# Optimization experiments

Hardware: AMD Instinct MI355X
Metric: run time of the kernel (lower is better)

Reference implementation:

```python
import jax, jax.numpy as jnp
import numpy as np

INPUT_DIM = 384
H1, H2, BOTTLENECK = 512, 216, 10
NUM_ANNOTATORS = 2316
BATCH = 16384


def setup_inputs() -> dict:
    key = jax.random.key(0)
    ks = jax.random.split(key, 9)

    def lin(k, fan_in, fan_out):
        # torch nn.Linear default init: U(-1/sqrt(fan_in), 1/sqrt(fan_in))
        bound = 1.0 / np.sqrt(fan_in)
        kw, kb = jax.random.split(k)
        W = jax.random.uniform(kw, (fan_in, fan_out), jnp.float32, -bound, bound)
        b = jax.random.uniform(kb, (fan_out,), jnp.float32, -bound, bound)
        return W, b

    x = jax.random.normal(ks[0], (BATCH, INPUT_DIM), jnp.float32)
    W1, b1 = lin(ks[1], INPUT_DIM, H1)
    W2, b2 = lin(ks[2], H1, H2)
    W3, b3 = lin(ks[3], H2, BOTTLENECK)
    # 2316 heads of Linear(10, 1) stacked into a single (10, 2316) matrix + (2316,) bias
    Wh, bh = lin(ks[4], BOTTLENECK, NUM_ANNOTATORS)
    return {"x": x, "W1": W1, "b1": b1, "W2": W2, "b2": b2,
            "W3": W3, "b3": b3, "Wh": Wh, "bh": bh}


def reference(x, W1, b1, W2, b2, W3, b3, Wh, bh):
    # shared encoder (dropout is identity in eval mode)
    h = jax.nn.relu(x @ W1 + b1)            # [B, 512]
    h = jax.nn.relu(h @ W2 + b2)            # [B, 216]
    f = jax.nn.relu(h @ W3 + b3)            # [B, 10]
    # 2316 per-annotator heads fused into one GEMM: [B,10] @ [10,2316] + [2316]
    return f @ Wh + bh                      # [B, 2316]
```

## Files before the change

### kernel.cpp

```cpp
#include <hip/hip_runtime.h>
#include <hip/hip_bf16.h>
#include <stdint.h>

using f32x4  = __attribute__((ext_vector_type(4))) float;
using bf16x8 = __attribute__((ext_vector_type(8))) __bf16;
using u16x4  = __attribute__((ext_vector_type(4))) unsigned short;
using u16x8  = __attribute__((ext_vector_type(8))) unsigned short;

#define DEVFN static __device__ __forceinline__

constexpr int IND = 384, N1 = 512, N2R = 216, N2 = 256, NB = 10, NA = 2316;
constexpr int BATCH = 16384;
constexpr int RB  = 64;
constexpr int NC1 = 12;
constexpr int NC2 = 16;
constexpr int K3  = 224;

constexpr int WS_W1  = 0;
constexpr int WS_W2  = WS_W1 + NC1 * N1 * 32;
constexpr int WS_W3  = WS_W2 + NC2 * N2 * 32;
constexpr size_t WS_NEED = 708864;

constexpr int XT_OFF = 0;      constexpr int XT_ST = 784;
constexpr int W1T    = 51200;
constexpr int H1_OFF = 0;      constexpr int H1_ST = 1040;
constexpr int W2T    = 66560;
constexpr int H2_OFF = 0;      constexpr int H2_ST = 528;
constexpr int W3_OFF = 115712;
constexpr int F_OFF  = 122880; constexpr int F_ST  = 48;
constexpr int B1L    = 149504;
constexpr int B2L    = 151552;
constexpr int B3L    = 152576;
constexpr int LDS_E  = 152640;

DEVFN unsigned short bf16u(float f) {
    __hip_bfloat16 h = __float2bfloat16(f);
    unsigned short u; __builtin_memcpy(&u, &h, 2); return u;
}

DEVFN void mfma16(f32x4& d, bf16x8 a, bf16x8 b) {
    d = __builtin_amdgcn_mfma_f32_16x16x32_bf16(a, b, d, 0, 0, 0);
}

DEVFN void gll16(const void* g, void* lds) {
    __builtin_amdgcn_global_load_lds((const __attribute__((address_space(1))) void*)g,
                                     (__attribute__((address_space(3))) void*)lds, 16, 0, 0);
}

DEVFN void wait_vm4()   { asm volatile("s_waitcnt vmcnt(4)" ::: "memory"); }
DEVFN void wait_vm2()   { asm volatile("s_waitcnt vmcnt(2)" ::: "memory"); }
DEVFN void wait_vm0()   { asm volatile("s_waitcnt vmcnt(0)" ::: "memory"); }
DEVFN void wait_lgkm0() { asm volatile("s_waitcnt lgkmcnt(0)" ::: "memory"); }

__global__ __launch_bounds__(256)
void cvt_weights(const float* __restrict__ W1, const float* __restrict__ W2,
                 const float* __restrict__ W3,
                 unsigned short* __restrict__ ws)
{
    const int bid = blockIdx.x, tid = threadIdx.x;
    if (bid < 48) {
        const int c = bid >> 2, o = bid & 3;
        #pragma unroll
        for (int half = 0; half < 2; ++half) {
            const int col = half * 256 + tid;
            u16x8 v;
            #pragma unroll
            for (int s7 = 0; s7 < 8; ++s7)
                v[s7] = bf16u(W1[(size_t)(c * 32 + o * 8 + s7) * N1 + col]);
            *(u16x8*)(ws + WS_W1 + c * 16384 + col * 32 + ((o ^ (col & 3)) << 3)) = v;
        }
    } else if (bid < 112) {
        const int t = bid - 48;
        const int c = t >> 2, o = t & 3;
        const int col = tid;
        u16x8 v;
        #pragma unroll
        for (int s7 = 0; s7 < 8; ++s7) {
            int k = c * 32 + o * 8 + s7;
            v[s7] = (col < N2R) ? bf16u(W2[(size_t)k * N2R + col]) : (unsigned short)0;
        }
        *(u16x8*)(ws + WS_W2 + c * 8192 + col * 32 + ((o ^ (col & 3)) << 3)) = v;
    } else {
        for (int i = tid; i < 16 * K3; i += 256) {
            int col = i / K3, s = i - col * K3;
            int sb = s >> 5, r = s & 31;
            int k = sb * 32 + (((r >> 3) ^ (col & 3)) << 3) + (r & 7);
            float v = (col < NB && k < 216) ? W3[k * NB + col] : 0.f;
            ws[WS_W3 + i] = bf16u(v);
        }
    }
}

__global__ __launch_bounds__(512)
void fused_mlp(const float* __restrict__ x,
               const float* __restrict__ b1g, const float* __restrict__ b2g,
               const float* __restrict__ b3g,
               const unsigned short* __restrict__ ws,
               const float* __restrict__ WhG, const float* __restrict__ bhg,
               float* __restrict__ out)
{
    __shared__ __attribute__((aligned(16))) unsigned char smem[LDS_E];
    const int tid  = threadIdx.x;
    const int wave = tid >> 6;
    const int lane = tid & 63;
    const int l16  = lane & 15;
    const int lk   = lane >> 4;
    const int wr   = wave >> 2;
    const int wc   = wave & 3;
    const int row0 = blockIdx.x * RB;

    const unsigned char* wsW1 = (const unsigned char*)(ws + WS_W1);
    const unsigned char* wsW2 = (const unsigned char*)(ws + WS_W2);

    #pragma unroll
    for (int cc = 0; cc < 2; ++cc)
        #pragma unroll
        for (int o = 0; o < 4; ++o) {
            int wb = o * 8192 + wave * 1024;
            gll16(wsW1 + cc * 32768 + wb + lane * 16, smem + W1T + cc * 32768 + wb);
        }

    {
        const float4* xg = (const float4*)(x + (size_t)row0 * IND);
        #pragma unroll
        for (int i = 0; i < 12; ++i) {
            int j = tid + i * 512;
            float4 v = xg[j];
            int el = j * 4, r = el / IND, c = el - r * IND;
            u16x4 h;
            h[0] = bf16u(v.x); h[1] = bf16u(v.y); h[2] = bf16u(v.z); h[3] = bf16u(v.w);
            *(u16x4*)(smem + XT_OFF + r * XT_ST + c * 2) = h;
        }
        *(float*)(smem + B1L + tid * 4) = b1g[tid];
        if (tid < 256) *(float*)(smem + B2L + tid * 4) = (tid < N2R) ? b2g[tid] : 0.f;
        if (tid < 16)  *(float*)(smem + B3L + tid * 4) = (tid < NB)  ? b3g[tid] : 0.f;
    }
    __syncthreads();

    f32x4 acc1[2][8] = {};

    for (int c = 0; c < NC1; ++c) {
        if (c + 1 < NC1) wait_vm4(); else wait_vm2();
        __builtin_amdgcn_s_barrier();
        if (c + 2 < NC1) {
            const unsigned char* src = wsW1 + (size_t)(c + 2) * 32768;
            const int nxt = W1T + ((c + 2) % 3) * 32768;
            #pragma unroll
            for (int o = 0; o < 4; ++o) {
                int wb = o * 8192 + wave * 1024;
                gll16(src + wb + lane * 16, smem + nxt + wb);
            }
        } else {
            const int cc = c - 10;
            #pragma unroll
            for (int o = 0; o < 2; ++o) {
                int wb = o * 8192 + wave * 1024;
                gll16(wsW2 + cc * 16384 + wb + lane * 16, smem + W2T + cc * 16384 + wb);
            }
        }
        const int cur = W1T + (c % 3) * 32768;
        const int k0 = c * 32;
        bf16x8 a0 = *(const bf16x8*)(smem + XT_OFF + (wr * 32 + l16)      * XT_ST + (k0 + lk * 8) * 2);
        bf16x8 a1 = *(const bf16x8*)(smem + XT_OFF + (wr * 32 + 16 + l16) * XT_ST + (k0 + lk * 8) * 2);
        #pragma unroll
        for (int n = 0; n < 8; ++n) {
            int col = wc * 128 + n * 16 + l16;
            bf16x8 b = *(const bf16x8*)(smem + cur + col * 64 + ((lk ^ (col & 3)) << 4));
            mfma16(acc1[0][n], a0, b);
            mfma16(acc1[1][n], a1, b);
        }
    }
    __builtin_amdgcn_s_barrier();
    #pragma unroll
    for (int m = 0; m < 2; ++m)
        #pragma unroll
        for (int n = 0; n < 8; ++n) {
            int col = wc * 128 + n * 16 + l16;
            float bias = *(const float*)(smem + B1L + col * 4);
            #pragma unroll
            for (int e = 0; e < 4; ++e) {
                float v = fmaxf(acc1[m][n][e] + bias, 0.f);
                *(unsigned short*)(smem + H1_OFF + (wr * 32 + m * 16 + lk * 4 + e) * H1_ST + col * 2) = bf16u(v);
            }
        }
    wait_lgkm0();
    __builtin_amdgcn_s_barrier();

    f32x4 acc2[2][4] = {};

    for (int c = 0; c < NC2; ++c) {
        if (c + 1 < NC2) wait_vm2(); else wait_vm0();
        __builtin_amdgcn_s_barrier();
        if (c + 2 < NC2) {
            const unsigned char* src = wsW2 + (size_t)(c + 2) * 16384;
            const int nxt = W2T + ((c + 2) % 3) * 16384;
            #pragma unroll
            for (int o = 0; o < 2; ++o) {
                int wb = o * 8192 + wave * 1024;
                gll16(src + wb + lane * 16, smem + nxt + wb);
            }
        }
        const int cur = W2T + (c % 3) * 16384;
        const int k0 = c * 32;
        bf16x8 a0 = *(const bf16x8*)(smem + H1_OFF + (wr * 32 + l16)      * H1_ST + (k0 + lk * 8) * 2);
        bf16x8 a1 = *(const bf16x8*)(smem + H1_OFF + (wr * 32 + 16 + l16) * H1_ST + (k0 + lk * 8) * 2);
        #pragma unroll
        for (int n = 0; n < 4; ++n) {
            int col = wc * 64 + n * 16 + l16;
            bf16x8 b = *(const bf16x8*)(smem + cur + col * 64 + ((lk ^ (col & 3)) << 4));
            mfma16(acc2[0][n], a0, b);
            mfma16(acc2[1][n], a1, b);
        }
    }

    const int j0 = tid;
    const int j1 = 512 + tid;
    const bool has1 = (j1 < 579);
    float w0[10][4], w1[10][4];
    float4 bh0 = ((const float4*)bhg)[j0];
    float4 bh1 = make_float4(0.f, 0.f, 0.f, 0.f);
    #pragma unroll
    for (int k = 0; k < 10; ++k) {
        f32x4 q = *(const f32x4*)(WhG + (size_t)k * NA + j0 * 4);
        w0[k][0] = q[0]; w0[k][1] = q[1]; w0[k][2] = q[2]; w0[k][3] = q[3];
    }
    if (has1) {
        #pragma unroll
        for (int k = 0; k < 10; ++k) {
            f32x4 q = *(const f32x4*)(WhG + (size_t)k * NA + j1 * 4);
            w1[k][0] = q[0]; w1[k][1] = q[1]; w1[k][2] = q[2]; w1[k][3] = q[3];
        }
        bh1 = ((const float4*)bhg)[j1];
    }

    __builtin_amdgcn_s_barrier();
    #pragma unroll
    for (int m = 0; m < 2; ++m)
        #pragma unroll
        for (int n = 0; n < 4; ++n) {
            int col = wc * 64 + n * 16 + l16;
            float bias = *(const float*)(smem + B2L + col * 4);
            #pragma unroll
            for (int e = 0; e < 4; ++e) {
                float v = fmaxf(acc2[m][n][e] + bias, 0.f);
                *(unsigned short*)(smem + H2_OFF + (wr * 32 + m * 16 + lk * 4 + e) * H2_ST + col * 2) = bf16u(v);
            }
        }
    if (wave < 7)
        gll16((const unsigned char*)(ws + WS_W3) + wave * 1024 + lane * 16, smem + W3_OFF + wave * 1024);
    __syncthreads();

    f32x4 acc3[2] = {};
    #pragma unroll
    for (int c = 0; c < 7; ++c) {
        const int k0 = c * 32;
        bf16x8 a0 = *(const bf16x8*)(smem + H2_OFF + (wr * 32 + l16)      * H2_ST + (k0 + lk * 8) * 2);
        bf16x8 a1 = *(const bf16x8*)(smem + H2_OFF + (wr * 32 + 16 + l16) * H2_ST + (k0 + lk * 8) * 2);
        bf16x8 b  = *(const bf16x8*)(smem + W3_OFF + l16 * 448 + c * 64 + ((lk ^ (l16 & 3)) << 4));
        mfma16(acc3[0], a0, b);
        mfma16(acc3[1], a1, b);
    }
    if (wc == 0 && l16 < NB) {
        float bias = *(const float*)(smem + B3L + l16 * 4);
        #pragma unroll
        for (int m = 0; m < 2; ++m)
            #pragma unroll
            for (int e = 0; e < 4; ++e) {
                float v = fmaxf(acc3[m][e] + bias, 0.f);
                *(float*)(smem + F_OFF + (wr * 32 + m * 16 + lk * 4 + e) * F_ST + l16 * 4) = v;
            }
    }
    __syncthreads();

    #pragma unroll 1
    for (int rg = 0; rg < 16; ++rg) {
        float fv[4][10];
        #pragma unroll
        for (int rr = 0; rr < 4; ++rr) {
            const unsigned char* fb = smem + F_OFF + (rg * 4 + rr) * F_ST;
            f32x4 p0 = *(const f32x4*)(fb);
            f32x4 p1 = *(const f32x4*)(fb + 16);
            float2 p2 = *(const float2*)(fb + 32);
            fv[rr][0] = p0[0]; fv[rr][1] = p0[1]; fv[rr][2] = p0[2]; fv[rr][3] = p0[3];
            fv[rr][4] = p1[0]; fv[rr][5] = p1[1]; fv[rr][6] = p1[2]; fv[rr][7] = p1[3];
            fv[rr][8] = p2.x;  fv[rr][9] = p2.y;
        }
        float ac[4][4];
        #pragma unroll
        for (int rr = 0; rr < 4; ++rr) {
            ac[rr][0] = bh0.x; ac[rr][1] = bh0.y; ac[rr][2] = bh0.z; ac[rr][3] = bh0.w;
            #pragma unroll
            for (int k = 0; k < 10; ++k) {
                ac[rr][0] = fmaf(fv[rr][k], w0[k][0], ac[rr][0]);
                ac[rr][1] = fmaf(fv[rr][k], w0[k][1], ac[rr][1]);
                ac[rr][2] = fmaf(fv[rr][k], w0[k][2], ac[rr][2]);
                ac[rr][3] = fmaf(fv[rr][k], w0[k][3], ac[rr][3]);
            }
        }
        #pragma unroll
        for (int rr = 0; rr < 4; ++rr) {
            float4 o;
            o.x = ac[rr][0]; o.y = ac[rr][1]; o.z = ac[rr][2]; o.w = ac[rr][3];
            *(float4*)(out + (size_t)(row0 + rg * 4 + rr) * NA + j0 * 4) = o;
        }
        if (has1) {
            float ac1[4][4];
            #pragma unroll
            for (int rr = 0; rr < 4; ++rr) {
                ac1[rr][0] = bh1.x; ac1[rr][1] = bh1.y; ac1[rr][2] = bh1.z; ac1[rr][3] = bh1.w;
                #pragma unroll
                for (int k = 0; k < 10; ++k) {
                    ac1[rr][0] = fmaf(fv[rr][k], w1[k][0], ac1[rr][0]);
                    ac1[rr][1] = fmaf(fv[rr][k], w1[k][1], ac1[rr][1]);
                    ac1[rr][2] = fmaf(fv[rr][k], w1[k][2], ac1[rr][2]);
                    ac1[rr][3] = fmaf(fv[rr][k], w1[k][3], ac1[rr][3]);
                }
            }
            #pragma unroll
            for (int rr = 0; rr < 4; ++rr) {
                float4 o;
                o.x = ac1[rr][0]; o.y = ac1[rr][1]; o.z = ac1[rr][2]; o.w = ac1[rr][3];
                *(float4*)(out + (size_t)(row0 + rg * 4 + rr) * NA + j1 * 4) = o;
            }
        }
    }
}

extern "C" void kernel_launch(void* const* d_in, const int* in_sizes, int n_in,
                              void* d_out, int out_size, void* d_ws, size_t ws_size,
                              hipStream_t stream)
{
    const float* x  = (const float*)d_in[0];
    const float* W1 = (const float*)d_in[1];
    const float* b1 = (const float*)d_in[2];
    const float* W2 = (const float*)d_in[3];
    const float* b2 = (const float*)d_in[4];
    const float* W3 = (const float*)d_in[5];
    const float* b3 = (const float*)d_in[6];
    const float* Wh = (const float*)d_in[7];
    const float* bh = (const float*)d_in[8];
    unsigned short* ws = (unsigned short*)d_ws;
    float* out = (float*)d_out;

    if (ws_size < WS_NEED) return;

    cvt_weights<<<dim3(113), dim3(256), 0, stream>>>(W1, W2, W3, ws);
    fused_mlp<<<dim3(BATCH / RB), dim3(512), 0, stream>>>(x, b1, b2, b3, ws, Wh, bh, out);
}
```

Baseline: 51.21 us.

## Retile layer-1 MFMA to 4x4 per wave and rebalance head tail columns

Layer-1 GEMM changes from a 2x8 tile per wave (32 rows by 128 cols) to a 4x4 tile (all 64 rows by 64 cols per wave). This balances A and B fragment loads from LDS per MFMA. The head output tail (columns 512..578) was computed by only 67 threads. It is now spread over all 512 threads across row groups, which removes the divergent second pass and its register-held weights. The cost is extra global reads of Wh for the tail work items.

Measured after the change: 50.26 us (median of 2 runs). Within noise of the previous version (-1.9%).

```diff
diff --git a/kernel.cpp b/kernel.cpp
--- a/kernel.cpp
+++ b/kernel.cpp
@@ -137,7 +137,7 @@
     }
     __syncthreads();
 
-    f32x4 acc1[2][8] = {};
+    f32x4 acc1[4][4] = {};
 
     for (int c = 0; c < NC1; ++c) {
         if (c + 1 < NC1) wait_vm4(); else wait_vm2();
@@ -160,27 +160,32 @@
         }
         const int cur = W1T + (c % 3) * 32768;
         const int k0 = c * 32;
-        bf16x8 a0 = *(const bf16x8*)(smem + XT_OFF + (wr * 32 + l16)      * XT_ST + (k0 + lk * 8) * 2);
-        bf16x8 a1 = *(const bf16x8*)(smem + XT_OFF + (wr * 32 + 16 + l16) * XT_ST + (k0 + lk * 8) * 2);
-        #pragma unroll
-        for (int n = 0; n < 8; ++n) {
-            int col = wc * 128 + n * 16 + l16;
-            bf16x8 b = *(const bf16x8*)(smem + cur + col * 64 + ((lk ^ (col & 3)) << 4));
-            mfma16(acc1[0][n], a0, b);
-            mfma16(acc1[1][n], a1, b);
-        }
+        bf16x8 a[4], b[4];
+        #pragma unroll
+        for (int m = 0; m < 4; ++m)
+            a[m] = *(const bf16x8*)(smem + XT_OFF + (m * 16 + l16) * XT_ST + (k0 + lk * 8) * 2);
+        #pragma unroll
+        for (int n = 0; n < 4; ++n) {
+            int col = wave * 64 + n * 16 + l16;
+            b[n] = *(const bf16x8*)(smem + cur + col * 64 + ((lk ^ (col & 3)) << 4));
+        }
+        #pragma unroll
+        for (int m = 0; m < 4; ++m)
+            #pragma unroll
+            for (int n = 0; n < 4; ++n)
+                mfma16(acc1[m][n], a[m], b[n]);
     }
     __builtin_amdgcn_s_barrier();
     #pragma unroll
-    for (int m = 0; m < 2; ++m)
-        #pragma unroll
-        for (int n = 0; n < 8; ++n) {
-            int col = wc * 128 + n * 16 + l16;
+    for (int m = 0; m < 4; ++m)
+        #pragma unroll
+        for (int n = 0; n < 4; ++n) {
+            int col = wave * 64 + n * 16 + l16;
             float bias = *(const float*)(smem + B1L + col * 4);
             #pragma unroll
             for (int e = 0; e < 4; ++e) {
                 float v = fmaxf(acc1[m][n][e] + bias, 0.f);
-                *(unsigned short*)(smem + H1_OFF + (wr * 32 + m * 16 + lk * 4 + e) * H1_ST + col * 2) = bf16u(v);
+                *(unsigned short*)(smem + H1_OFF + (m * 16 + lk * 4 + e) * H1_ST + col * 2) = bf16u(v);
             }
         }
     wait_lgkm0();
@@ -214,23 +219,12 @@
     }
 
     const int j0 = tid;
-    const int j1 = 512 + tid;
-    const bool has1 = (j1 < 579);
-    float w0[10][4], w1[10][4];
+    float w0[10][4];
     float4 bh0 = ((const float4*)bhg)[j0];
-    float4 bh1 = make_float4(0.f, 0.f, 0.f, 0.f);
     #pragma unroll
     for (int k = 0; k < 10; ++k) {
         f32x4 q = *(const f32x4*)(WhG + (size_t)k * NA + j0 * 4);
         w0[k][0] = q[0]; w0[k][1] = q[1]; w0[k][2] = q[2]; w0[k][3] = q[3];
-    }
-    if (has1) {
-        #pragma unroll
-        for (int k = 0; k < 10; ++k) {
-            f32x4 q = *(const f32x4*)(WhG + (size_t)k * NA + j1 * 4);
-            w1[k][0] = q[0]; w1[k][1] = q[1]; w1[k][2] = q[2]; w1[k][3] = q[3];
-        }
-        bh1 = ((const float4*)bhg)[j1];
     }
 
     __builtin_amdgcn_s_barrier();
@@ -303,25 +297,43 @@
             o.x = ac[rr][0]; o.y = ac[rr][1]; o.z = ac[rr][2]; o.w = ac[rr][3];
             *(float4*)(out + (size_t)(row0 + rg * 4 + rr) * NA + j0 * 4) = o;
         }
-        if (has1) {
-            float ac1[4][4];
-            #pragma unroll
-            for (int rr = 0; rr < 4; ++rr) {
-                ac1[rr][0] = bh1.x; ac1[rr][1] = bh1.y; ac1[rr][2] = bh1.z; ac1[rr][3] = bh1.w;
-                #pragma unroll
-                for (int k = 0; k < 10; ++k) {
-                    ac1[rr][0] = fmaf(fv[rr][k], w1[k][0], ac1[rr][0]);
-                    ac1[rr][1] = fmaf(fv[rr][k], w1[k][1], ac1[rr][1]);
-                    ac1[rr][2] = fmaf(fv[rr][k], w1[k][2], ac1[rr][2]);
-                    ac1[rr][3] = fmaf(fv[rr][k], w1[k][3], ac1[rr][3]);
-                }
-            }
-            #pragma unroll
-            for (int rr = 0; rr < 4; ++rr) {
-                float4 o;
-                o.x = ac1[rr][0]; o.y = ac1[rr][1]; o.z = ac1[rr][2]; o.w = ac1[rr][3];
-                *(float4*)(out + (size_t)(row0 + rg * 4 + rr) * NA + j1 * 4) = o;
-            }
+    }
+
+    #pragma unroll 1
+    for (int idx = tid; idx < 67 * 16; idx += 512) {
+        const int q  = idx % 67;
+        const int rg = idx / 67;
+        const int jq = 512 + q;
+        float4 bhv = ((const float4*)bhg)[jq];
+        float wt[10][4];
+        #pragma unroll
+        for (int k = 0; k < 10; ++k) {
+            f32x4 qv = *(const f32x4*)(WhG + (size_t)k * NA + jq * 4);
+            wt[k][0] = qv[0]; wt[k][1] = qv[1]; wt[k][2] = qv[2]; wt[k][3] = qv[3];
+        }
+        float fv[4][10];
+        #pragma unroll
+        for (int rr = 0; rr < 4; ++rr) {
+            const unsigned char* fb = smem + F_OFF + (rg * 4 + rr) * F_ST;
+            f32x4 p0 = *(const f32x4*)(fb);
+            f32x4 p1 = *(const f32x4*)(fb + 16);
+            float2 p2 = *(const float2*)(fb + 32);
+            fv[rr][0] = p0[0]; fv[rr][1] = p0[1]; fv[rr][2] = p0[2]; fv[rr][3] = p0[3];
+            fv[rr][4] = p1[0]; fv[rr][5] = p1[1]; fv[rr][6] = p1[2]; fv[rr][7] = p1[3];
+            fv[rr][8] = p2.x;  fv[rr][9] = p2.y;
+        }
+        #pragma unroll
+        for (int rr = 0; rr < 4; ++rr) {
+            float a0 = bhv.x, a1 = bhv.y, a2 = bhv.z, a3 = bhv.w;
+            #pragma unroll
+            for (int k = 0; k < 10; ++k) {
+                a0 = fmaf(fv[rr][k], wt[k][0], a0);
+                a1 = fmaf(fv[rr][k], wt[k][1], a1);
+                a2 = fmaf(fv[rr][k], wt[k][2], a2);
+                a3 = fmaf(fv[rr][k], wt[k][3], a3);
+            }
+            float4 o; o.x = a0; o.y = a1; o.z = a2; o.w = a3;
+            *(float4*)(out + (size_t)(row0 + rg * 4 + rr) * NA + jq * 4) = o;
         }
     }
 }
```
